# Kernel tuning notes

Measured on AMD Instinct MI355X. Metric: run time of the kernel, lower is better.

Reference implementation:

```python
import jax, jax.numpy as jnp
import numpy as np

B, T, D = 2, 1024, 1024
H, DH = 16, 64          # d_head = d_model // n_heads
MAX_POS = 64


def setup_inputs() -> dict:
    key = jax.random.key(0)
    ks = jax.random.split(key, 11)
    s = 1.0 / np.sqrt(D)
    x = jax.random.normal(ks[0], (B, T, D), jnp.float32)
    Wq = jax.random.normal(ks[1], (D, D), jnp.float32) * s
    Wk = jax.random.normal(ks[2], (D, D), jnp.float32) * s
    Wv = jax.random.normal(ks[3], (D, D), jnp.float32) * s
    Wo = jax.random.normal(ks[4], (D, D), jnp.float32) * s
    bq = jnp.zeros((D,), jnp.float32)
    bk = jnp.zeros((D,), jnp.float32)
    bv = jnp.zeros((D,), jnp.float32)
    bo = jnp.zeros((D,), jnp.float32)
    pos_emb = jax.random.normal(ks[5], (H, MAX_POS, DH), jnp.float32) * 0.02
    causal_mask = jnp.triu(jnp.ones((T, T), bool), k=1)  # True = masked (j > i)
    return dict(x=x, Wq=Wq, bq=bq, Wk=Wk, bk=bk, Wv=Wv, bv=bv, Wo=Wo, bo=bo,
                pos_emb=pos_emb, causal_mask=causal_mask)


def reference(x, Wq, bq, Wk, bk, Wv, bv, Wo, bo, pos_emb, causal_mask):
    Bv, Tv, _ = x.shape
    scale = np.sqrt(DH).astype(np.float32)

    def proj(W, b):
        return (x @ W.T + b).reshape(Bv, Tv, H, DH).transpose(0, 2, 1, 3)  # (B,H,T,d)

    Q, K, V = proj(Wq, bq), proj(Wk, bk), proj(Wv, bv)

    qk = jnp.einsum('bhid,bhjd->bhij', Q, K)              # (B,H,T,T)
    gates = jax.nn.sigmoid(qk / scale)
    gates = jnp.where(causal_mask, 0.0, gates)
    cum = jnp.cumsum(gates, axis=-1)
    pos = cum[..., -1:] - cum                             # total - cumsum_left

    pos = jnp.clip(pos, 0.0, MAX_POS - 1.0)
    pos_floor = jnp.floor(pos)
    alpha = (pos - pos_floor)[..., None]                  # (B,H,T,T,1) -> broadcast
    fidx = pos_floor.astype(jnp.int32)
    cidx = jnp.clip(jnp.ceil(pos), 0, MAX_POS - 1).astype(jnp.int32)

    # q_i . PE_{i,j} via precomputed q.pos_emb table (same math, no (B,H,T,T,d) tensor)
    qpe_tab = jnp.einsum('bhid,hpd->bhip', Q, pos_emb)    # (B,H,T,MAX_POS)
    qpe_f = jnp.take_along_axis(qpe_tab, fidx, axis=-1)   # (B,H,T,T)
    qpe_c = jnp.take_along_axis(qpe_tab, cidx, axis=-1)
    q_pe = (1.0 - alpha[..., 0]) * qpe_f + alpha[..., 0] * qpe_c

    scores = (qk + q_pe) / scale
    scores = jnp.where(causal_mask, -jnp.inf, scores)
    attn = jax.nn.softmax(scores, axis=-1)

    out = jnp.einsum('bhij,bhjd->bhid', attn, V)
    out = out.transpose(0, 2, 1, 3).reshape(Bv, Tv, D)
    return out @ Wo.T + bo
```

## Files before the change

kernel.cpp:

```cpp
#include <hip/hip_runtime.h>
#include <math.h>

#define Tt 1024
#define Dd 1024
#define Hh 16
#define DHh 64
#define MAXPOS 64
#define BTt 2048

typedef short short8 __attribute__((ext_vector_type(8)));
typedef float floatx4 __attribute__((ext_vector_type(4)));

#define MFMA16 __builtin_amdgcn_mfma_f32_16x16x32_bf16

__device__ __forceinline__ unsigned short f2bf(float f) {
    unsigned u;
    __builtin_memcpy(&u, &f, 4);
    u = (u + 0x7FFFu + ((u >> 16) & 1u)) >> 16;
    return (unsigned short)u;
}
__device__ __forceinline__ float bf2fs(short s) {
    unsigned u = ((unsigned)(unsigned short)s) << 16;
    float f;
    __builtin_memcpy(&f, &u, 4);
    return f;
}
__device__ __forceinline__ float fsigm(float x) {
    return __builtin_amdgcn_rcpf(1.f + __expf(-x));
}
__device__ __forceinline__ void gl2lds16(const short* __restrict__ g, short* l) {
    __builtin_amdgcn_global_load_lds(
        (const __attribute__((address_space(1))) void*)g,
        (__attribute__((address_space(3))) void*)l,
        16, 0, 0);
}

__global__ __launch_bounds__(256) void conv_bf16(
    const float* __restrict__ x,  const float* __restrict__ W0,
    const float* __restrict__ W1, const float* __restrict__ W2,
    const float* __restrict__ W3,
    short* __restrict__ xb, short* __restrict__ w0b, short* __restrict__ w1b,
    short* __restrict__ w2b, short* __restrict__ w3b)
{
    const float* src; short* dst; int n;
    switch (blockIdx.y) {
        case 0:  src = x;  dst = xb;  n = BTt * Dd; break;
        case 1:  src = W0; dst = w0b; n = Dd * Dd;  break;
        case 2:  src = W1; dst = w1b; n = Dd * Dd;  break;
        case 3:  src = W2; dst = w2b; n = Dd * Dd;  break;
        default: src = W3; dst = w3b; n = Dd * Dd;  break;
    }
    int idx = (blockIdx.x * 256 + threadIdx.x) * 8;
    if (idx >= n) return;
    floatx4 a0 = *(const floatx4*)&src[idx];
    floatx4 a1 = *(const floatx4*)&src[idx + 4];
    short8 s;
    for (int e = 0; e < 4; ++e) {
        s[e]     = (short)f2bf(a0[e]);
        s[e + 4] = (short)f2bf(a1[e]);
    }
    *(short8*)&dst[idx] = s;
}

template <int MODE, int TMW>
__device__ __forceinline__ void gemm_body(const short* __restrict__ A,
                                          const short* __restrict__ W,
                                          const float* __restrict__ bias,
                                          void* __restrict__ Cout,
                                          int N, int K)
{
    __shared__ __align__(16) short Ash[2][TMW * 64 * 64];
    __shared__ __align__(16) short Bsh[2][64 * 64];
    const int t = threadIdx.x;
    const int lane = t & 63, wave = t >> 6;
    const int quad = lane >> 4, l16 = lane & 15;
    const int row0 = blockIdx.x * (TMW * 64), col0 = blockIdx.y * 64;

    const int g_r = lane >> 3, g_c = (lane & 7) * 8;

    floatx4 acc[TMW][4];
    for (int a = 0; a < TMW; ++a)
        for (int b2 = 0; b2 < 4; ++b2)
            acc[a][b2] = (floatx4){0.f, 0.f, 0.f, 0.f};

#define STAGE(buf, kb)                                                      \
    do {                                                                    \
        for (int i = 0; i < TMW * 2; ++i) {                                 \
            int rbase = (wave * (TMW * 2) + i) * 8;                         \
            gl2lds16(&A[(size_t)(row0 + rbase + g_r) * K + (kb) + g_c],     \
                     &Ash[buf][rbase * 64]);                                \
        }                                                                   \
        for (int i = 0; i < 2; ++i) {                                       \
            int rbase = (wave * 2 + i) * 8;                                 \
            gl2lds16(&W[(size_t)(col0 + rbase + g_r) * K + (kb) + g_c],     \
                     &Bsh[buf][rbase * 64]);                                \
        }                                                                   \
    } while (0)

    const int NT = K / 64;
    STAGE(0, 0);
    __syncthreads();
    for (int ts = 0; ts < NT; ++ts) {
        const int cur = ts & 1;
        if (ts + 1 < NT) STAGE(cur ^ 1, (ts + 1) * 64);
        for (int ks = 0; ks < 2; ++ks) {
            short8 af[TMW], bfr[4];
            for (int tm = 0; tm < TMW; ++tm)
                af[tm] = *(short8*)&Ash[cur][(wave * (TMW * 16) + tm * 16 + l16) * 64 + ks * 32 + quad * 8];
            for (int tn = 0; tn < 4; ++tn)
                bfr[tn] = *(short8*)&Bsh[cur][(tn * 16 + l16) * 64 + ks * 32 + quad * 8];
            for (int tm = 0; tm < TMW; ++tm)
                for (int tn = 0; tn < 4; ++tn)
                    acc[tm][tn] = MFMA16(af[tm], bfr[tn], acc[tm][tn], 0, 0, 0);
        }
        if (ts + 1 < NT) __syncthreads();
    }
#undef STAGE
    for (int tm = 0; tm < TMW; ++tm)
        for (int tn = 0; tn < 4; ++tn) {
            int col = col0 + tn * 16 + l16;
            float bv = bias[col];
            for (int r = 0; r < 4; ++r) {
                int row = row0 + wave * (TMW * 16) + tm * 16 + quad * 4 + r;
                float v = acc[tm][tn][r] + bv;
                if (MODE == 0) ((float*)Cout)[(size_t)row * N + col] = v;
                else           ((short*)Cout)[(size_t)row * N + col] = (short)f2bf(v);
            }
        }
}

__global__ __launch_bounds__(256) void gemm_qkv(
    const short* __restrict__ xb,
    const short* __restrict__ Wqb, const short* __restrict__ Wkb,
    const short* __restrict__ Wvb,
    const float* __restrict__ bq, const float* __restrict__ bk,
    const float* __restrict__ bv,
    short* __restrict__ Qb, short* __restrict__ Kb, short* __restrict__ Vrow)
{
    if (blockIdx.z == 0)      gemm_body<1, 2>(xb, Wqb, bq, Qb, Dd, Dd);
    else if (blockIdx.z == 1) gemm_body<1, 2>(xb, Wkb, bk, Kb, Dd, Dd);
    else                      gemm_body<1, 2>(xb, Wvb, bv, Vrow, Dd, Dd);
}

__global__ __launch_bounds__(256) void gemm_o(
    const short* __restrict__ A, const short* __restrict__ W,
    const float* __restrict__ bias, float* __restrict__ C)
{
    gemm_body<0, 1>(A, W, bias, C, Dd, Dd);
}

__global__ __launch_bounds__(256) void v_transpose(
    const short* __restrict__ Vrow, short* __restrict__ Vt)
{
    __shared__ __align__(16) short L[64 * 72];
    const int t = threadIdx.x;
    const int j0 = blockIdx.x * 64, d0 = blockIdx.y * 64, b = blockIdx.z;
    for (int s = 0; s < 2; ++s) {
        int c = t * 2 + s;
        int jr = c >> 3, c8 = c & 7;
        *(short8*)&L[jr * 72 + c8 * 8] =
            *(const short8*)&Vrow[((size_t)(b * Tt + j0 + jr)) * Dd + d0 + c8 * 8];
    }
    __syncthreads();
    for (int s = 0; s < 2; ++s) {
        int c = t * 2 + s;
        int dr = c >> 3, c8 = c & 7;
        short8 v;
        for (int e = 0; e < 8; ++e) v[e] = L[(c8 * 8 + e) * 72 + dr];
        *(short8*)&Vt[((size_t)(b * Dd + d0 + dr)) * Tt + j0 + c8 * 8] = v;
    }
}

__device__ __constant__ int ITMAP[32] = {
     0,  1,  2,  3,  8,  9, 10, 11,
    28, 29, 30, 31, 20, 21, 22, 23,
     4,  5,  6,  7, 12, 13, 14, 15,
    24, 25, 26, 27, 16, 17, 18, 19};

__global__ __launch_bounds__(256) void cope_attn(
    const short* __restrict__ Q, const short* __restrict__ K,
    const short* __restrict__ Vt, const float* __restrict__ PE,
    short* __restrict__ AOb)
{
    const int h = blockIdx.x & 15, b = blockIdx.x >> 4;
    const int it = ITMAP[blockIdx.y];
    const int i0 = it * 32;
    const int t = threadIdx.x, lane = t & 63, wave = t >> 6;
    const int quad = lane >> 4, l16 = lane & 15;

    __shared__ __align__(16) short SldS[32 * 264];
    __shared__ __align__(16) short KV[128 * 72];
    __shared__ short qpeB[32 * 68];
    __shared__ float lrow[32];
    float* Sld = (float*)SldS;

    const float inv_scale = 0.125f;
    const int sr = t >> 3, ss = t & 7;
    const int irow = i0 + sr;

    short* QtS = SldS;
    {
        int r = t >> 3, c = t & 7;
        *(short8*)&QtS[r * 72 + c * 8] =
            *(const short8*)&Q[((size_t)(b * Tt + i0 + r)) * Dd + h * DHh + c * 8];
    }
    for (int e = 0; e < 16; ++e) {
        int idx = t + 256 * e;
        int p = idx >> 6, d = idx & 63;
        KV[p * 72 + d] = (short)f2bf(PE[((size_t)h * MAXPOS + p) * DHh + d]);
    }
    __syncthreads();

    short8 qa[2][2];
    for (int rb = 0; rb < 2; ++rb)
        for (int ks = 0; ks < 2; ++ks)
            qa[rb][ks] = *(short8*)&QtS[(rb * 16 + l16) * 72 + ks * 32 + quad * 8];

    {
        int mt = wave >> 1;
        int ntA = 2 * (wave & 1), ntB = ntA + 1;
        floatx4 c0f = {0, 0, 0, 0}, c1f = {0, 0, 0, 0};
        for (int ks = 0; ks < 2; ++ks) {
            short8 b0 = *(short8*)&KV[(ntA * 16 + l16) * 72 + ks * 32 + quad * 8];
            short8 b1 = *(short8*)&KV[(ntB * 16 + l16) * 72 + ks * 32 + quad * 8];
            c0f = MFMA16(qa[mt][ks], b0, c0f, 0, 0, 0);
            c1f = MFMA16(qa[mt][ks], b1, c1f, 0, 0, 0);
        }
        for (int r = 0; r < 4; ++r) {
            qpeB[(mt * 16 + quad * 4 + r) * 68 + ntA * 16 + l16] = (short)f2bf(c0f[r]);
            qpeB[(mt * 16 + quad * 4 + r) * 68 + ntB * 16 + l16] = (short)f2bf(c1f[r]);
        }
    }

    const int JT = (i0 + 159) >> 7;
    floatx4 o0 = {0, 0, 0, 0}, o1 = {0, 0, 0, 0};
    const int pv_mt = wave >> 1;
    const int pv_ntA = 2 * (wave & 1), pv_ntB = pv_ntA + 1;
    float l_acc = 0.f;
    float rightAcc = 0.f;

    short8 kreg[4];
    for (int e = 0; e < 4; ++e) {
        int ch = t + 256 * e;
        int jr = ch >> 3, c = ch & 7;
        kreg[e] = *(const short8*)&K[((size_t)(b * Tt + (JT - 1) * 128 + jr)) * Dd + h * DHh + c * 8];
    }

    for (int jt = JT - 1; jt >= 0; --jt) {
        const int j0 = jt * 128;
        __syncthreads();
        for (int e = 0; e < 4; ++e) {
            int ch = t + 256 * e;
            int jr = ch >> 3, c = ch & 7;
            *(short8*)&KV[jr * 72 + c * 8] = kreg[e];
        }
        __syncthreads();
        short8 vreg[4];
        for (int e = 0; e < 4; ++e) {
            int ch = t + 256 * e;
            int d = ch >> 4, c = ch & 15;
            vreg[e] = *(const short8*)&Vt[((size_t)(b * Dd + h * DHh + d)) * Tt + j0 + c * 8];
        }
        if (jt > 0) {
            for (int e = 0; e < 4; ++e) {
                int ch = t + 256 * e;
                int jr = ch >> 3, c = ch & 7;
                kreg[e] = *(const short8*)&K[((size_t)(b * Tt + j0 - 128 + jr)) * Dd + h * DHh + c * 8];
            }
        }
        {
            int ntA = 2 * wave, ntB = ntA + 1;
            floatx4 c00 = {0,0,0,0}, c01 = {0,0,0,0}, c10 = {0,0,0,0}, c11 = {0,0,0,0};
            for (int ks = 0; ks < 2; ++ks) {
                short8 b0 = *(short8*)&KV[(ntA * 16 + l16) * 72 + ks * 32 + quad * 8];
                short8 b1 = *(short8*)&KV[(ntB * 16 + l16) * 72 + ks * 32 + quad * 8];
                c00 = MFMA16(qa[0][ks], b0, c00, 0, 0, 0);
                c01 = MFMA16(qa[0][ks], b1, c01, 0, 0, 0);
                c10 = MFMA16(qa[1][ks], b0, c10, 0, 0, 0);
                c11 = MFMA16(qa[1][ks], b1, c11, 0, 0, 0);
            }
            for (int r = 0; r < 4; ++r) {
                Sld[(quad * 4 + r) * 132 + ntA * 16 + l16] = c00[r];
                Sld[(quad * 4 + r) * 132 + ntB * 16 + l16] = c01[r];
                Sld[(16 + quad * 4 + r) * 132 + ntA * 16 + l16] = c10[r];
                Sld[(16 + quad * 4 + r) * 132 + ntB * 16 + l16] = c11[r];
            }
        }
        __syncthreads();
        {
            floatx4 qv[4];
            for (int q4 = 0; q4 < 4; ++q4) {
                short8 qraw = *(short8*)&SldS[sr * 264 + ss * 32 + q4 * 8];
                __builtin_memcpy(&qv[q4], &qraw, 16);
            }
            float gt[16];
            float gs = 0.f;
            for (int e = 0; e < 16; ++e) {
                int j = j0 + ss * 16 + e;
                float qk = qv[e >> 2][e & 3];
                float g = (j <= irow) ? fsigm(qk * inv_scale) : 0.f;
                gt[e] = g;
                gs += g;
            }
            float inc = gs;
            for (int d2 = 1; d2 < 8; d2 <<= 1) {
                float n = __shfl_down(inc, d2, 64);
                if ((lane & 7) + d2 < 8) inc += n;
            }
            float tileTot = __shfl(inc, lane & 56, 64);
            float base = rightAcc + (inc - gs);
            float run = 0.f;
            short8 p0, p1;
            for (int e = 15; e >= 0; --e) {
                int j = j0 + ss * 16 + e;
                float pos = base + run;
                run += gt[e];
                pos = fminf(fmaxf(pos, 0.f), 63.f);
                float pf = floorf(pos);
                float al = pos - pf;
                int fi = (int)pf;
                int ci = fi + 1; if (ci > 63) ci = 63;
                float qp = (1.f - al) * bf2fs(qpeB[sr * 68 + fi]) + al * bf2fs(qpeB[sr * 68 + ci]);
                float qk = qv[e >> 2][e & 3];
                float p = (j <= irow) ? __expf((qk + qp) * inv_scale) : 0.f;
                if (e < 8) p0[e] = (short)f2bf(p); else p1[e - 8] = (short)f2bf(p);
                l_acc += p;
            }
            *(short8*)&SldS[sr * 264 + ss * 32]     = p0;
            *(short8*)&SldS[sr * 264 + ss * 32 + 8] = p1;
            rightAcc += tileTot;
        }
        for (int e = 0; e < 4; ++e) {
            int ch = t + 256 * e;
            int d = ch >> 4, c = ch & 15;
            *(short8*)&KV[d * 136 + c * 8] = vreg[e];
        }
        __syncthreads();
        for (int ks = 0; ks < 4; ++ks) {
            short8 a  = *(short8*)&SldS[(pv_mt * 16 + l16) * 264 + ks * 64
                                        + ((quad >> 1) << 5) + ((quad & 1) << 3)];
            short8 b0 = *(short8*)&KV[(pv_ntA * 16 + l16) * 136 + ks * 32 + quad * 8];
            short8 b1 = *(short8*)&KV[(pv_ntB * 16 + l16) * 136 + ks * 32 + quad * 8];
            o0 = MFMA16(a, b0, o0, 0, 0, 0);
            o1 = MFMA16(a, b1, o1, 0, 0, 0);
        }
    }
    float lr = l_acc;
    for (int d2 = 4; d2 >= 1; d2 >>= 1) lr += __shfl_xor(lr, d2, 64);
    if (ss == 0) lrow[sr] = lr;
    __syncthreads();
    for (int r = 0; r < 4; ++r) {
        int row = pv_mt * 16 + quad * 4 + r;
        float inv = __builtin_amdgcn_rcpf(lrow[row]);
        size_t off = ((size_t)(b * Tt + i0 + row)) * Dd + h * DHh;
        AOb[off + pv_ntA * 16 + l16] = (short)f2bf(o0[r] * inv);
        AOb[off + pv_ntB * 16 + l16] = (short)f2bf(o1[r] * inv);
    }
}

extern "C" void kernel_launch(void* const* d_in, const int* in_sizes, int n_in,
                              void* d_out, int out_size, void* d_ws, size_t ws_size,
                              hipStream_t stream)
{
    const float* x  = (const float*)d_in[0];
    const float* Wq = (const float*)d_in[1];
    const float* bq = (const float*)d_in[2];
    const float* Wk = (const float*)d_in[3];
    const float* bk = (const float*)d_in[4];
    const float* Wv = (const float*)d_in[5];
    const float* bv = (const float*)d_in[6];
    const float* Wo = (const float*)d_in[7];
    const float* bo = (const float*)d_in[8];
    const float* pe = (const float*)d_in[9];

    short* xb   = (short*)d_ws;
    short* Wqb  = xb   + (size_t)BTt * Dd;
    short* Wkb  = Wqb  + (size_t)Dd * Dd;
    short* Wvb  = Wkb  + (size_t)Dd * Dd;
    short* Wob  = Wvb  + (size_t)Dd * Dd;
    short* Qb   = Wob  + (size_t)Dd * Dd;
    short* Kb   = Qb   + (size_t)BTt * Dd;
    short* Vrow = Kb   + (size_t)BTt * Dd;
    short* Vtg  = Vrow + (size_t)BTt * Dd;
    short* AOb  = Vtg  + (size_t)BTt * Dd;

    dim3 gc(BTt * Dd / 8 / 256, 5);
    conv_bf16<<<gc, 256, 0, stream>>>(x, Wq, Wk, Wv, Wo, xb, Wqb, Wkb, Wvb, Wob);

    dim3 gq(BTt / 128, Dd / 64, 3);
    gemm_qkv<<<gq, 256, 0, stream>>>(xb, Wqb, Wkb, Wvb, bq, bk, bv, Qb, Kb, Vrow);

    dim3 gv(Tt / 64, Dd / 64, 2);
    v_transpose<<<gv, 256, 0, stream>>>(Vrow, Vtg);

    dim3 ga(32, 32, 1);
    cope_attn<<<ga, 256, 0, stream>>>(Qb, Kb, Vtg, pe, AOb);

    dim3 go(BTt / 64, Dd / 64, 1);
    gemm_o<<<go, 256, 0, stream>>>(AOb, Wob, bo, (float*)d_out);
}
```

Before: 177.6 us.

## Split K/V shared buffers to drop a barrier and reorder tile scheduling

Splits the shared K/V staging buffer into separate K and V buffers. The next K tile can then be written to LDS right after the QK MFMA barrier, which removes two __syncthreads per iteration, and the K prefetch is moved one tile further ahead. The ITMAP block order is also permuted so heavy causal tiles are dispatched first. The cost is extra LDS (about 17 KB), which could lower occupancy.

Result: slower. 184.5 us (+3.9%).

```diff
diff --git a/kernel.cpp b/kernel.cpp
--- a/kernel.cpp
+++ b/kernel.cpp
@@ -172,10 +172,10 @@
 }
 
 __device__ __constant__ int ITMAP[32] = {
+    28, 29, 30, 31, 20, 21, 22, 23,
      0,  1,  2,  3,  8,  9, 10, 11,
-    28, 29, 30, 31, 20, 21, 22, 23,
-     4,  5,  6,  7, 12, 13, 14, 15,
-    24, 25, 26, 27, 16, 17, 18, 19};
+    24, 25, 26, 27, 16, 17, 18, 19,
+     4,  5,  6,  7, 12, 13, 14, 15};
 
 __global__ __launch_bounds__(256) void cope_attn(
     const short* __restrict__ Q, const short* __restrict__ K,
@@ -189,7 +189,8 @@
     const int quad = lane >> 4, l16 = lane & 15;
 
     __shared__ __align__(16) short SldS[32 * 264];
-    __shared__ __align__(16) short KV[128 * 72];
+    __shared__ __align__(16) short Kbl[128 * 72];
+    __shared__ __align__(16) short Vbl[64 * 136];
     __shared__ short qpeB[32 * 68];
     __shared__ float lrow[32];
     float* Sld = (float*)SldS;
@@ -207,7 +208,7 @@
     for (int e = 0; e < 16; ++e) {
         int idx = t + 256 * e;
         int p = idx >> 6, d = idx & 63;
-        KV[p * 72 + d] = (short)f2bf(PE[((size_t)h * MAXPOS + p) * DHh + d]);
+        Kbl[p * 72 + d] = (short)f2bf(PE[((size_t)h * MAXPOS + p) * DHh + d]);
     }
     __syncthreads();
 
@@ -215,14 +216,23 @@
     for (int rb = 0; rb < 2; ++rb)
         for (int ks = 0; ks < 2; ++ks)
             qa[rb][ks] = *(short8*)&QtS[(rb * 16 + l16) * 72 + ks * 32 + quad * 8];
+
+    const int JT = (i0 + 159) >> 7;
+
+    short8 kreg[4];
+    for (int e = 0; e < 4; ++e) {
+        int ch = t + 256 * e;
+        int jr = ch >> 3, c = ch & 7;
+        kreg[e] = *(const short8*)&K[((size_t)(b * Tt + (JT - 1) * 128 + jr)) * Dd + h * DHh + c * 8];
+    }
 
     {
         int mt = wave >> 1;
         int ntA = 2 * (wave & 1), ntB = ntA + 1;
         floatx4 c0f = {0, 0, 0, 0}, c1f = {0, 0, 0, 0};
         for (int ks = 0; ks < 2; ++ks) {
-            short8 b0 = *(short8*)&KV[(ntA * 16 + l16) * 72 + ks * 32 + quad * 8];
-            short8 b1 = *(short8*)&KV[(ntB * 16 + l16) * 72 + ks * 32 + quad * 8];
+            short8 b0 = *(short8*)&Kbl[(ntA * 16 + l16) * 72 + ks * 32 + quad * 8];
+            short8 b1 = *(short8*)&Kbl[(ntB * 16 + l16) * 72 + ks * 32 + quad * 8];
             c0f = MFMA16(qa[mt][ks], b0, c0f, 0, 0, 0);
             c1f = MFMA16(qa[mt][ks], b1, c1f, 0, 0, 0);
         }
@@ -231,49 +241,42 @@
             qpeB[(mt * 16 + quad * 4 + r) * 68 + ntB * 16 + l16] = (short)f2bf(c1f[r]);
         }
     }
-
-    const int JT = (i0 + 159) >> 7;
+    __syncthreads();
+
+    for (int e = 0; e < 4; ++e) {
+        int ch = t + 256 * e;
+        int jr = ch >> 3, c = ch & 7;
+        *(short8*)&Kbl[jr * 72 + c * 8] = kreg[e];
+    }
+    if (JT > 1) {
+        for (int e = 0; e < 4; ++e) {
+            int ch = t + 256 * e;
+            int jr = ch >> 3, c = ch & 7;
+            kreg[e] = *(const short8*)&K[((size_t)(b * Tt + (JT - 2) * 128 + jr)) * Dd + h * DHh + c * 8];
+        }
+    }
+    __syncthreads();
+
     floatx4 o0 = {0, 0, 0, 0}, o1 = {0, 0, 0, 0};
     const int pv_mt = wave >> 1;
     const int pv_ntA = 2 * (wave & 1), pv_ntB = pv_ntA + 1;
     float l_acc = 0.f;
     float rightAcc = 0.f;
 
-    short8 kreg[4];
-    for (int e = 0; e < 4; ++e) {
-        int ch = t + 256 * e;
-        int jr = ch >> 3, c = ch & 7;
-        kreg[e] = *(const short8*)&K[((size_t)(b * Tt + (JT - 1) * 128 + jr)) * Dd + h * DHh + c * 8];
-    }
-
     for (int jt = JT - 1; jt >= 0; --jt) {
         const int j0 = jt * 128;
-        __syncthreads();
-        for (int e = 0; e < 4; ++e) {
-            int ch = t + 256 * e;
-            int jr = ch >> 3, c = ch & 7;
-            *(short8*)&KV[jr * 72 + c * 8] = kreg[e];
-        }
-        __syncthreads();
         short8 vreg[4];
         for (int e = 0; e < 4; ++e) {
             int ch = t + 256 * e;
             int d = ch >> 4, c = ch & 15;
             vreg[e] = *(const short8*)&Vt[((size_t)(b * Dd + h * DHh + d)) * Tt + j0 + c * 8];
         }
-        if (jt > 0) {
-            for (int e = 0; e < 4; ++e) {
-                int ch = t + 256 * e;
-                int jr = ch >> 3, c = ch & 7;
-                kreg[e] = *(const short8*)&K[((size_t)(b * Tt + j0 - 128 + jr)) * Dd + h * DHh + c * 8];
-            }
-        }
         {
             int ntA = 2 * wave, ntB = ntA + 1;
             floatx4 c00 = {0,0,0,0}, c01 = {0,0,0,0}, c10 = {0,0,0,0}, c11 = {0,0,0,0};
             for (int ks = 0; ks < 2; ++ks) {
-                short8 b0 = *(short8*)&KV[(ntA * 16 + l16) * 72 + ks * 32 + quad * 8];
-                short8 b1 = *(short8*)&KV[(ntB * 16 + l16) * 72 + ks * 32 + quad * 8];
+                short8 b0 = *(short8*)&Kbl[(ntA * 16 + l16) * 72 + ks * 32 + quad * 8];
+                short8 b1 = *(short8*)&Kbl[(ntB * 16 + l16) * 72 + ks * 32 + quad * 8];
                 c00 = MFMA16(qa[0][ks], b0, c00, 0, 0, 0);
                 c01 = MFMA16(qa[0][ks], b1, c01, 0, 0, 0);
                 c10 = MFMA16(qa[1][ks], b0, c10, 0, 0, 0);
@@ -287,6 +290,20 @@
             }
         }
         __syncthreads();
+        if (jt > 0) {
+            for (int e = 0; e < 4; ++e) {
+                int ch = t + 256 * e;
+                int jr = ch >> 3, c = ch & 7;
+                *(short8*)&Kbl[jr * 72 + c * 8] = kreg[e];
+            }
+            if (jt > 1) {
+                for (int e = 0; e < 4; ++e) {
+                    int ch = t + 256 * e;
+                    int jr = ch >> 3, c = ch & 7;
+                    kreg[e] = *(const short8*)&K[((size_t)(b * Tt + j0 - 256 + jr)) * Dd + h * DHh + c * 8];
+                }
+            }
+        }
         {
             floatx4 qv[4];
             for (int q4 = 0; q4 < 4; ++q4) {
@@ -333,14 +350,14 @@
         for (int e = 0; e < 4; ++e) {
             int ch = t + 256 * e;
             int d = ch >> 4, c = ch & 15;
-            *(short8*)&KV[d * 136 + c * 8] = vreg[e];
+            *(short8*)&Vbl[d * 136 + c * 8] = vreg[e];
         }
         __syncthreads();
         for (int ks = 0; ks < 4; ++ks) {
             short8 a  = *(short8*)&SldS[(pv_mt * 16 + l16) * 264 + ks * 64
                                         + ((quad >> 1) << 5) + ((quad & 1) << 3)];
-            short8 b0 = *(short8*)&KV[(pv_ntA * 16 + l16) * 136 + ks * 32 + quad * 8];
-            short8 b1 = *(short8*)&KV[(pv_ntB * 16 + l16) * 136 + ks * 32 + quad * 8];
+            short8 b0 = *(short8*)&Vbl[(pv_ntA * 16 + l16) * 136 + ks * 32 + quad * 8];
+            short8 b1 = *(short8*)&Vbl[(pv_ntB * 16 + l16) * 136 + ks * 32 + quad * 8];
             o0 = MFMA16(a, b0, o0, 0, 0, 0);
             o1 = MFMA16(a, b1, o1, 0, 0, 0);
         }
```
